# Optimization experiments

Measured on AMD Instinct MI355X. Metric: run time of the kernel, lower is better.

Reference implementation:

```python
import jax, jax.numpy as jnp
import numpy as np

L = 4        # num decoder layers
H = 8        # heads
D = 512      # d_model
DFF = 2048   # ffn hidden
V = 8000     # target vocab
B = 16       # batch
S_ENC = 128  # encoder seq len
T = 32       # decode target_length
START, END, NULL = 1, 2, 0
NEG = -1e9
EPS = 1e-6


def sinusoid_pos(max_len, d):
    pos = np.arange(max_len)[:, None].astype(np.float32)
    i = np.arange(d)[None, :].astype(np.float32)
    ang = pos / np.power(10000.0, (2.0 * np.floor(i / 2.0)) / d)
    pe = np.where(np.arange(d)[None, :] % 2 == 0, np.sin(ang), np.cos(ang))
    return jnp.asarray(pe[None], jnp.float32)  # [1, max_len, d]


def setup_inputs() -> dict:
    key = jax.random.key(0)
    ks = jax.random.split(key, 16)
    g = lambda k, shape: jax.random.normal(k, shape, jnp.float32) * 0.02
    return {
        "target_length": T,
        "encoder_output": jax.random.normal(ks[0], (B, S_ENC, D), jnp.float32),
        "padding_mask": jnp.zeros((B, S_ENC), jnp.float32),  # 1.0 where padded
        "embed": g(ks[1], (V, D)),
        "wq": g(ks[2], (L, D, D)), "wk": g(ks[3], (L, D, D)),
        "wv": g(ks[4], (L, D, D)), "wo": g(ks[5], (L, D, D)),
        "cwq": g(ks[6], (L, D, D)), "cwk": g(ks[7], (L, D, D)),
        "cwv": g(ks[8], (L, D, D)), "cwo": g(ks[9], (L, D, D)),
        "w1": g(ks[10], (L, D, DFF)), "b1": jnp.zeros((L, DFF), jnp.float32),
        "w2": g(ks[11], (L, DFF, D)), "b2": jnp.zeros((L, D), jnp.float32),
        "ln_g": jnp.ones((L, 3, D), jnp.float32), "ln_b": jnp.zeros((L, 3, D), jnp.float32),
        "fc_w": g(ks[12], (D, V)), "fc_b": jnp.zeros((V,), jnp.float32),
    }


def ln(x, g, b):
    m = jnp.mean(x, axis=-1, keepdims=True)
    v = jnp.mean(jnp.square(x - m), axis=-1, keepdims=True)
    return (x - m) * jax.lax.rsqrt(v + EPS) * g + b


def mha(q_in, kv_in, wq, wk, wv, wo, mask):
    Bn, Sq, d = q_in.shape
    dh = d // H
    q = (q_in @ wq).reshape(Bn, Sq, H, dh)
    k = (kv_in @ wk).reshape(Bn, -1, H, dh)
    v = (kv_in @ wv).reshape(Bn, -1, H, dh)
    s = jnp.einsum('bqhd,bkhd->bhqk', q, k) / jnp.sqrt(jnp.float32(dh)) + mask
    a = jax.nn.softmax(s, axis=-1)
    o = jnp.einsum('bhqk,bkhd->bqhd', a, v).reshape(Bn, Sq, d)
    return o @ wo


def decoder_stack(x, encoder_output, self_mask, cross_mask,
                  wq, wk, wv, wo, cwq, cwk, cwv, cwo,
                  w1, b1, w2, b2, ln_g, ln_b):
    for i in range(L):
        a = mha(x, x, wq[i], wk[i], wv[i], wo[i], self_mask)
        x = ln(x + a, ln_g[i, 0], ln_b[i, 0])
        a2 = mha(x, encoder_output, cwq[i], cwk[i], cwv[i], cwo[i], cross_mask)
        x = ln(x + a2, ln_g[i, 1], ln_b[i, 1])
        f = jax.nn.relu(x @ w1[i] + b1[i]) @ w2[i] + b2[i]
        x = ln(x + f, ln_g[i, 2], ln_b[i, 2])
    return x


def reference(target_length, encoder_output, padding_mask, embed,
              wq, wk, wv, wo, cwq, cwk, cwv, cwo,
              w1, b1, w2, b2, ln_g, ln_b, fc_w, fc_b):
    Bn, S, d = encoder_output.shape
    Tp1 = target_length + 1
    pos_enc = sinusoid_pos(Tp1, d)
    sqrt_d = jnp.sqrt(jnp.float32(d))
    cross_mask = padding_mask[:, None, None, :] * NEG  # [B,1,1,S_enc]
    tokens0 = jnp.full((Bn, Tp1), NULL, jnp.int32).at[:, 0].set(START)
    done0 = jnp.zeros((Bn,), bool)

    def step(carry, t):
        tokens, done = carry
        # re-embed the whole (fixed-size, masked) prefix buffer each step
        x = embed[tokens] * sqrt_d + pos_enc
        # only positions <= t are valid keys; no look-ahead mask (matches original)
        self_mask = jnp.where(jnp.arange(Tp1) <= t, 0.0, NEG)[None, None, None, :]
        x = decoder_stack(x, encoder_output, self_mask, cross_mask,
                          wq, wk, wv, wo, cwq, cwk, cwv, cwo,
                          w1, b1, w2, b2, ln_g, ln_b)
        out = x[:, t, :] @ fc_w + fc_b  # logits at last valid position
        max_idx = jnp.argmax(out, axis=-1).astype(jnp.int32)
        done = done | (max_idx == END)
        tok = jnp.where(done, jnp.int32(NULL), max_idx)
        tokens = tokens.at[:, t + 1].set(tok)
        return (tokens, done), None

    (tokens, done), _ = jax.lax.scan(step, (tokens0, done0), jnp.arange(target_length))
    return tokens[:, 1:].astype(jnp.int64)
```

## Files before the change

### kernel.cpp

```cpp
#include <hip/hip_runtime.h>
#include <math.h>

#define L_   4
#define H_   8
#define D_   512
#define DH   64
#define DFF_ 2048
#define V_   8000
#define B_   16
#define SENC 128
#define T_   32
#define TP1  33
#define NEGV -1e9f
#define EPSV 1e-6f
#define SQRTD 22.627416997969522f
#define XSZ  ((size_t)TP1 * B_ * D_)

__global__ __launch_bounds__(256) void gemm32_k(
    const float* __restrict__ A, const float* __restrict__ W,
    const float* __restrict__ bias, float* __restrict__ C,
    int M, int N, int K, int kchunk, size_t pstride, int relu, int tmode)
{
    __shared__ __align__(16) float As[2][16][34];
    __shared__ __align__(16) float Bs[2][16][68];
    int tid = threadIdx.x;
    int tx = tid & 15, ty = tid >> 4;
    int m0 = blockIdx.y * 32, n0 = blockIdx.x * 64;
    int kbeg = blockIdx.z * kchunk;
    int niter = kchunk >> 4;
    C += (size_t)blockIdx.z * pstride;
    int am = tid >> 2, aseg = tid & 3;
    int bk = tid >> 4, bc4 = (tid & 15) * 4;
    float4 aReg = make_float4(0.f, 0.f, 0.f, 0.f), bReg;
    {
        int k0 = kbeg;
        if (tid < 128) {
            int gm = m0 + am;
            if (gm < M) aReg = *(const float4*)&A[(size_t)gm * K + k0 + aseg * 4];
        }
        bReg = *(const float4*)&W[(size_t)(k0 + bk) * N + n0 + bc4];
    }
    if (tid < 128) {
        As[0][aseg * 4 + 0][am] = aReg.x;
        As[0][aseg * 4 + 1][am] = aReg.y;
        As[0][aseg * 4 + 2][am] = aReg.z;
        As[0][aseg * 4 + 3][am] = aReg.w;
    }
    *(float4*)&Bs[0][bk][bc4] = bReg;
    __syncthreads();
    float acc[2][4] = {};
    for (int it = 0; it < niter; it++) {
        int cur = it & 1;
        if (it + 1 < niter) {
            int k0 = kbeg + (it + 1) * 16;
            if (tid < 128) {
                int gm = m0 + am;
                aReg = make_float4(0.f, 0.f, 0.f, 0.f);
                if (gm < M) aReg = *(const float4*)&A[(size_t)gm * K + k0 + aseg * 4];
            }
            bReg = *(const float4*)&W[(size_t)(k0 + bk) * N + n0 + bc4];
        }
        #pragma unroll
        for (int kk = 0; kk < 16; kk++) {
            float2 a2 = *(const float2*)&As[cur][kk][ty * 2];
            float4 b4 = *(const float4*)&Bs[cur][kk][tx * 4];
            acc[0][0] += a2.x * b4.x; acc[0][1] += a2.x * b4.y;
            acc[0][2] += a2.x * b4.z; acc[0][3] += a2.x * b4.w;
            acc[1][0] += a2.y * b4.x; acc[1][1] += a2.y * b4.y;
            acc[1][2] += a2.y * b4.z; acc[1][3] += a2.y * b4.w;
        }
        if (it + 1 < niter) {
            int nxt = 1 - cur;
            if (tid < 128) {
                As[nxt][aseg * 4 + 0][am] = aReg.x;
                As[nxt][aseg * 4 + 1][am] = aReg.y;
                As[nxt][aseg * 4 + 2][am] = aReg.z;
                As[nxt][aseg * 4 + 3][am] = aReg.w;
            }
            *(float4*)&Bs[nxt][bk][bc4] = bReg;
        }
        __syncthreads();
    }
    #pragma unroll
    for (int i = 0; i < 2; i++) {
        int gm = m0 + ty * 2 + i;
        if (gm >= M) continue;
        #pragma unroll
        for (int j = 0; j < 4; j++) {
            int gn = n0 + tx * 4 + j;
            float vv = acc[i][j];
            if (bias) vv += bias[gn];
            if (relu) vv = fmaxf(vv, 0.f);
            if (tmode == 1)
                C[(size_t)(gm >> 7) * 65536 + (size_t)gn * SENC + (gm & 127)] = vv;
            else
                C[(size_t)gm * N + gn] = vv;
        }
    }
}

__global__ __launch_bounds__(256) void gemm_qkv_k(
    const float* __restrict__ A, const float* __restrict__ W0,
    const float* __restrict__ W1, const float* __restrict__ W2,
    float* __restrict__ Cb, int M)
{
    __shared__ __align__(16) float As[2][16][34];
    __shared__ __align__(16) float Bs[2][16][68];
    int sel = blockIdx.x >> 3;
    const float* W = (sel == 0) ? W0 : ((sel == 1) ? W1 : W2);
    float* C = Cb + (size_t)sel * XSZ;
    int tid = threadIdx.x;
    int tx = tid & 15, ty = tid >> 4;
    int m0 = blockIdx.y * 32, n0 = (blockIdx.x & 7) * 64;
    int am = tid >> 2, aseg = tid & 3;
    int bk = tid >> 4, bc4 = (tid & 15) * 4;
    float4 aReg = make_float4(0.f, 0.f, 0.f, 0.f), bReg;
    {
        if (tid < 128) {
            int gm = m0 + am;
            if (gm < M) aReg = *(const float4*)&A[(size_t)gm * D_ + aseg * 4];
        }
        bReg = *(const float4*)&W[(size_t)bk * D_ + n0 + bc4];
    }
    if (tid < 128) {
        As[0][aseg * 4 + 0][am] = aReg.x;
        As[0][aseg * 4 + 1][am] = aReg.y;
        As[0][aseg * 4 + 2][am] = aReg.z;
        As[0][aseg * 4 + 3][am] = aReg.w;
    }
    *(float4*)&Bs[0][bk][bc4] = bReg;
    __syncthreads();
    float acc[2][4] = {};
    for (int it = 0; it < 32; it++) {
        int cur = it & 1;
        if (it + 1 < 32) {
            int k0 = (it + 1) * 16;
            if (tid < 128) {
                int gm = m0 + am;
                aReg = make_float4(0.f, 0.f, 0.f, 0.f);
                if (gm < M) aReg = *(const float4*)&A[(size_t)gm * D_ + k0 + aseg * 4];
            }
            bReg = *(const float4*)&W[(size_t)(k0 + bk) * D_ + n0 + bc4];
        }
        #pragma unroll
        for (int kk = 0; kk < 16; kk++) {
            float2 a2 = *(const float2*)&As[cur][kk][ty * 2];
            float4 b4 = *(const float4*)&Bs[cur][kk][tx * 4];
            acc[0][0] += a2.x * b4.x; acc[0][1] += a2.x * b4.y;
            acc[0][2] += a2.x * b4.z; acc[0][3] += a2.x * b4.w;
            acc[1][0] += a2.y * b4.x; acc[1][1] += a2.y * b4.y;
            acc[1][2] += a2.y * b4.z; acc[1][3] += a2.y * b4.w;
        }
        if (it + 1 < 32) {
            int nxt = 1 - cur;
            if (tid < 128) {
                As[nxt][aseg * 4 + 0][am] = aReg.x;
                As[nxt][aseg * 4 + 1][am] = aReg.y;
                As[nxt][aseg * 4 + 2][am] = aReg.z;
                As[nxt][aseg * 4 + 3][am] = aReg.w;
            }
            *(float4*)&Bs[nxt][bk][bc4] = bReg;
        }
        __syncthreads();
    }
    #pragma unroll
    for (int i = 0; i < 2; i++) {
        int gm = m0 + ty * 2 + i;
        if (gm >= M) continue;
        #pragma unroll
        for (int j = 0; j < 4; j++) {
            int gn = n0 + tx * 4 + j;
            if (sel == 1)
                C[(size_t)(gm & 15) * 16896 + (size_t)gn * TP1 + (gm >> 4)] =
                    acc[i][j];
            else
                C[(size_t)gm * D_ + gn] = acc[i][j];
        }
    }
}

__global__ void init_k(int* __restrict__ tokens, int* __restrict__ done,
                       float* __restrict__ cmask, const float* __restrict__ pm)
{
    int tid = threadIdx.x + blockIdx.x * 256;
    if (tid < B_ * TP1) tokens[tid] = ((tid % TP1) == 0) ? 1 : 0;
    if (tid < B_) done[tid] = 0;
    if (tid < B_ * SENC) cmask[tid] = pm[tid] * NEGV;
}

__global__ __launch_bounds__(256) void pe_k(float* __restrict__ pe)
{
    int p = blockIdx.x;
    for (int d = threadIdx.x; d < D_; d += 256) {
        float fd = (float)(2 * (d / 2)) / (float)D_;
        float ang = (float)p / powf(10000.f, fd);
        pe[(size_t)p * D_ + d] = (d & 1) ? cosf(ang) : sinf(ang);
    }
}

__global__ __launch_bounds__(256) void embed_k(
    const float* __restrict__ embed, int* __restrict__ tokens,
    float* __restrict__ x, const float* __restrict__ pe,
    const float* __restrict__ cand_v, const int* __restrict__ cand_i,
    int* __restrict__ done, int t)
{
    int p = blockIdx.x;
    int b = blockIdx.y;
    int tid = threadIdx.x;
    __shared__ float sv[128];
    __shared__ int si[128];
    __shared__ int stok;
    if (p == t && t > 0) {
        if (tid < 128) {
            float val = -1e30f; int idx = 0x7fffffff;
            if (tid < 125) {
                val = cand_v[(size_t)b * 125 + tid];
                idx = cand_i[(size_t)b * 125 + tid];
            }
            sv[tid] = val; si[tid] = idx;
        }
        __syncthreads();
        for (int s = 64; s; s >>= 1) {
            if (tid < s) {
                float ov = sv[tid + s]; int oi = si[tid + s];
                if (ov > sv[tid] || (ov == sv[tid] && oi < si[tid])) {
                    sv[tid] = ov; si[tid] = oi;
                }
            }
            __syncthreads();
        }
        if (tid == 0) {
            int best = si[0];
            int dn = done[b] | (best == 2 ? 1 : 0);
            done[b] = dn;
            int tk = dn ? 0 : best;
            tokens[b * TP1 + t] = tk;
            stok = tk;
        }
        __syncthreads();
    }
    int tok = (p == t && t > 0) ? stok : tokens[b * TP1 + p];
    const float* e = embed + (size_t)tok * D_;
    const float* pr = pe + (size_t)p * D_;
    float* xr = x + ((size_t)p * B_ + b) * D_;
    int c0 = tid * 2;
    float2 ev = *(const float2*)&e[c0];
    float2 pv = *(const float2*)&pr[c0];
    float2 o;
    o.x = ev.x * SQRTD + pv.x;
    o.y = ev.y * SQRTD + pv.y;
    *(float2*)&xr[c0] = o;
}

__device__ __forceinline__ float block_sum(float s) {
    __shared__ float red[4];
    #pragma unroll
    for (int off = 32; off; off >>= 1) s += __shfl_xor(s, off);
    if ((threadIdx.x & 63) == 0) red[threadIdx.x >> 6] = s;
    __syncthreads();
    float tot = red[0] + red[1] + red[2] + red[3];
    __syncthreads();
    return tot;
}

__device__ __forceinline__ float4 block_sum4(float4 s) {
    __shared__ __align__(16) float red4[4][4];
    #pragma unroll
    for (int off = 32; off; off >>= 1) {
        s.x += __shfl_xor(s.x, off);
        s.y += __shfl_xor(s.y, off);
        s.z += __shfl_xor(s.z, off);
        s.w += __shfl_xor(s.w, off);
    }
    if ((threadIdx.x & 63) == 0) *(float4*)red4[threadIdx.x >> 6] = s;
    __syncthreads();
    float4 t;
    t.x = red4[0][0] + red4[1][0] + red4[2][0] + red4[3][0];
    t.y = red4[0][1] + red4[1][1] + red4[2][1] + red4[3][1];
    t.z = red4[0][2] + red4[1][2] + red4[2][2] + red4[3][2];
    t.w = red4[0][3] + red4[1][3] + red4[2][3] + red4[3][3];
    __syncthreads();
    return t;
}

__global__ __launch_bounds__(256) void attn_mega_k(
    const float* __restrict__ q, const float* __restrict__ kT,
    const float* __restrict__ v, const float* __restrict__ wo,
    const float* __restrict__ KcT, const float* __restrict__ Vc,
    const float* __restrict__ cmask, const float* __restrict__ cwq,
    const float* __restrict__ cwo, float* __restrict__ x,
    const float* __restrict__ lg, const float* __restrict__ lb, int P)
{
    int b = blockIdx.x;
    int p0 = blockIdx.y * 4;
    int tid = threadIdx.x;
    int c0 = tid * 2;
    __shared__ float xs[4][D_];
    __shared__ float arow[4][D_];
    __shared__ float scs[4][H_][SENC + 4];
    __shared__ float inv[4][H_];
    #pragma unroll
    for (int g = 0; g < 4; g++) {
        float2 qv = make_float2(0.f, 0.f);
        if (p0 + g < P)
            qv = *(const float2*)&q[((size_t)(p0 + g) * B_ + b) * D_ + c0];
        *(float2*)&arow[g][c0] = qv;
    }
    __syncthreads();
    {
        int h = tid >> 5, kp = tid & 31;
        float a0 = 0.f, a1 = 0.f, a2 = 0.f, a3 = 0.f;
        if (kp < P) {
            const float* kb = kT + ((size_t)(b * 8 + h) * 64) * TP1 + kp;
            #pragma unroll 8
            for (int d = 0; d < 64; d++) {
                float kv = kb[(size_t)d * TP1];
                a0 += arow[0][h * 64 + d] * kv;
                a1 += arow[1][h * 64 + d] * kv;
                a2 += arow[2][h * 64 + d] * kv;
                a3 += arow[3][h * 64 + d] * kv;
            }
        }
        scs[0][h][kp] = a0 * 0.125f;
        scs[1][h][kp] = a1 * 0.125f;
        scs[2][h][kp] = a2 * 0.125f;
        scs[3][h][kp] = a3 * 0.125f;
    }
    __syncthreads();
    {
        int gh = tid >> 3, lane8 = tid & 7;
        int g = gh >> 3, h = gh & 7;
        float mx = -1e30f;
        for (int j = lane8; j < P; j += 8) mx = fmaxf(mx, scs[g][h][j]);
        mx = fmaxf(mx, __shfl_xor(mx, 1));
        mx = fmaxf(mx, __shfl_xor(mx, 2));
        mx = fmaxf(mx, __shfl_xor(mx, 4));
        float sum = 0.f;
        for (int j = lane8; j < P; j += 8) {
            float e = expf(scs[g][h][j] - mx);
            scs[g][h][j] = e;
            sum += e;
        }
        sum += __shfl_xor(sum, 1);
        sum += __shfl_xor(sum, 2);
        sum += __shfl_xor(sum, 4);
        if (lane8 == 0) inv[g][h] = 1.f / sum;
    }
    __syncthreads();
    {
        int h = tid >> 5;
        float o0[4] = {0.f, 0.f, 0.f, 0.f}, o1[4] = {0.f, 0.f, 0.f, 0.f};
        for (int j = 0; j < P; j++) {
            float2 vv = *(const float2*)&v[((size_t)j * B_ + b) * D_ + c0];
            #pragma unroll
            for (int g = 0; g < 4; g++) {
                float w = scs[g][h][j];
                o0[g] += w * vv.x; o1[g] += w * vv.y;
            }
        }
        #pragma unroll
        for (int g = 0; g < 4; g++) {
            arow[g][c0]     = o0[g] * inv[g][h];
            arow[g][c0 + 1] = o1[g] * inv[g][h];
        }
    }
    __syncthreads();
    {
        float v0[4], v1[4];
        #pragma unroll
        for (int g = 0; g < 4; g++) {
            float2 xv = make_float2(0.f, 0.f);
            if (p0 + g < P)
                xv = *(const float2*)&x[((size_t)(p0 + g) * B_ + b) * D_ + c0];
            v0[g] = xv.x; v1[g] = xv.y;
        }
        #pragma unroll 8
        for (int k = 0; k < D_; k++) {
            float2 wv = *(const float2*)&wo[(size_t)k * D_ + c0];
            #pragma unroll
            for (int g = 0; g < 4; g++) {
                float a = arow[g][k];
                v0[g] += a * wv.x; v1[g] += a * wv.y;
            }
        }
        float4 s1 = make_float4(v0[0] + v1[0], v0[1] + v1[1],
                                v0[2] + v1[2], v0[3] + v1[3]);
        float4 m4 = block_sum4(s1);
        float mean[4] = {m4.x * (1.f / 512.f), m4.y * (1.f / 512.f),
                         m4.z * (1.f / 512.f), m4.w * (1.f / 512.f)};
        float d0[4], d1[4];
        #pragma unroll
        for (int g = 0; g < 4; g++) {
            d0[g] = v0[g] - mean[g]; d1[g] = v1[g] - mean[g];
        }
        float4 s2 = make_float4(d0[0] * d0[0] + d1[0] * d1[0],
                                d0[1] * d0[1] + d1[1] * d1[1],
                                d0[2] * d0[2] + d1[2] * d1[2],
                                d0[3] * d0[3] + d1[3] * d1[3]);
        float4 w4 = block_sum4(s2);
        float var[4] = {w4.x * (1.f / 512.f), w4.y * (1.f / 512.f),
                        w4.z * (1.f / 512.f), w4.w * (1.f / 512.f)};
        float g0 = lg[c0], g1 = lg[c0 + 1];
        float bb0 = lb[c0], bb1 = lb[c0 + 1];
        #pragma unroll
        for (int g = 0; g < 4; g++) {
            float rs = rsqrtf(var[g] + EPSV);
            xs[g][c0]     = d0[g] * rs * g0 + bb0;
            xs[g][c0 + 1] = d1[g] * rs * g1 + bb1;
        }
    }
    __syncthreads();
    {
        float q0[4] = {0.f, 0.f, 0.f, 0.f}, q1[4] = {0.f, 0.f, 0.f, 0.f};
        #pragma unroll 8
        for (int k = 0; k < D_; k++) {
            float2 wv = *(const float2*)&cwq[(size_t)k * D_ + c0];
            #pragma unroll
            for (int g = 0; g < 4; g++) {
                float a = xs[g][k];
                q0[g] += a * wv.x; q1[g] += a * wv.y;
            }
        }
        #pragma unroll
        for (int g = 0; g < 4; g++) {
            arow[g][c0] = q0[g]; arow[g][c0 + 1] = q1[g];
        }
    }
    __syncthreads();
    #pragma unroll
    for (int i = 0; i < 4; i++) {
        int idx = tid + i * 256;
        int h = idx >> 7, s = idx & 127;
        const float* kb = KcT + ((size_t)(b * 512 + h * 64)) * SENC + s;
        float a0 = 0.f, a1 = 0.f, a2 = 0.f, a3 = 0.f;
        #pragma unroll 8
        for (int d = 0; d < 64; d++) {
            float kc = kb[(size_t)d * SENC];
            a0 += arow[0][h * 64 + d] * kc;
            a1 += arow[1][h * 64 + d] * kc;
            a2 += arow[2][h * 64 + d] * kc;
            a3 += arow[3][h * 64 + d] * kc;
        }
        float cm = cmask[b * SENC + s];
        scs[0][h][s] = a0 * 0.125f + cm;
        scs[1][h][s] = a1 * 0.125f + cm;
        scs[2][h][s] = a2 * 0.125f + cm;
        scs[3][h][s] = a3 * 0.125f + cm;
    }
    __syncthreads();
    {
        int gh = tid >> 3, lane8 = tid & 7;
        int g = gh >> 3, h = gh & 7;
        float mx = -1e30f;
        for (int s = lane8; s < SENC; s += 8) mx = fmaxf(mx, scs[g][h][s]);
        mx = fmaxf(mx, __shfl_xor(mx, 1));
        mx = fmaxf(mx, __shfl_xor(mx, 2));
        mx = fmaxf(mx, __shfl_xor(mx, 4));
        float sum = 0.f;
        for (int s = lane8; s < SENC; s += 8) {
            float e = expf(scs[g][h][s] - mx);
            scs[g][h][s] = e;
            sum += e;
        }
        sum += __shfl_xor(sum, 1);
        sum += __shfl_xor(sum, 2);
        sum += __shfl_xor(sum, 4);
        if (lane8 == 0) inv[g][h] = 1.f / sum;
    }
    __syncthreads();
    {
        int h = tid >> 5;
        float o0[4] = {0.f, 0.f, 0.f, 0.f}, o1[4] = {0.f, 0.f, 0.f, 0.f};
        for (int s = 0; s < SENC; s++) {
            float2 vv = *(const float2*)&Vc[((size_t)b * SENC + s) * D_ + c0];
            #pragma unroll
            for (int g = 0; g < 4; g++) {
                float w = scs[g][h][s];
                o0[g] += w * vv.x; o1[g] += w * vv.y;
            }
        }
        #pragma unroll
        for (int g = 0; g < 4; g++) {
            arow[g][c0]     = o0[g] * inv[g][h];
            arow[g][c0 + 1] = o1[g] * inv[g][h];
        }
    }
    __syncthreads();
    {
        float v0[4], v1[4];
        #pragma unroll
        for (int g = 0; g < 4; g++) {
            v0[g] = xs[g][c0]; v1[g] = xs[g][c0 + 1];
        }
        #pragma unroll 8
        for (int k = 0; k < D_; k++) {
            float2 wv = *(const float2*)&cwo[(size_t)k * D_ + c0];
            #pragma unroll
            for (int g = 0; g < 4; g++) {
                float a = arow[g][k];
                v0[g] += a * wv.x; v1[g] += a * wv.y;
            }
        }
        float4 s1 = make_float4(v0[0] + v1[0], v0[1] + v1[1],
                                v0[2] + v1[2], v0[3] + v1[3]);
        float4 m4 = block_sum4(s1);
        float mean[4] = {m4.x * (1.f / 512.f), m4.y * (1.f / 512.f),
                         m4.z * (1.f / 512.f), m4.w * (1.f / 512.f)};
        float d0[4], d1[4];
        #pragma unroll
        for (int g = 0; g < 4; g++) {
            d0[g] = v0[g] - mean[g]; d1[g] = v1[g] - mean[g];
        }
        float4 s2 = make_float4(d0[0] * d0[0] + d1[0] * d1[0],
                                d0[1] * d0[1] + d1[1] * d1[1],
                                d0[2] * d0[2] + d1[2] * d1[2],
                                d0[3] * d0[3] + d1[3] * d1[3]);
        float4 w4 = block_sum4(s2);
        float var[4] = {w4.x * (1.f / 512.f), w4.y * (1.f / 512.f),
                        w4.z * (1.f / 512.f), w4.w * (1.f / 512.f)};
        float g0 = lg[D_ + c0], g1 = lg[D_ + c0 + 1];
        float bb0 = lb[D_ + c0], bb1 = lb[D_ + c0 + 1];
        #pragma unroll
        for (int g = 0; g < 4; g++) {
            if (p0 + g < P) {
                float rs = rsqrtf(var[g] + EPSV);
                float* xr = x + ((size_t)(p0 + g) * B_ + b) * D_;
                xr[c0]     = d0[g] * rs * g0 + bb0;
                xr[c0 + 1] = d1[g] * rs * g1 + bb1;
            }
        }
    }
}

__global__ __launch_bounds__(256) void ln_red_k(
    float* __restrict__ x, const float* __restrict__ parts, size_t pstride,
    int nparts, const float* __restrict__ bias,
    const float* __restrict__ gam, const float* __restrict__ bet)
{
    int r = blockIdx.x;
    float* xr = x + (size_t)r * D_;
    int tid = threadIdx.x;
    float v0 = xr[tid];
    float v1 = xr[tid + 256];
    for (int s = 0; s < nparts; s++) {
        const float* pr = parts + (size_t)s * pstride + (size_t)r * D_;
        v0 += pr[tid];
        v1 += pr[tid + 256];
    }
    if (bias) { v0 += bias[tid]; v1 += bias[tid + 256]; }
    float mean = block_sum(v0 + v1) * (1.f / 512.f);
    float d0 = v0 - mean, d1 = v1 - mean;
    float var = block_sum(d0 * d0 + d1 * d1) * (1.f / 512.f);
    float rs = rsqrtf(var + EPSV);
    xr[tid]       = d0 * rs * gam[tid] + bet[tid];
    xr[tid + 256] = d1 * rs * gam[tid + 256] + bet[tid + 256];
}

__global__ __launch_bounds__(256) void logits_k(
    const float* __restrict__ x, const float* __restrict__ fcw,
    const float* __restrict__ fcb, float* __restrict__ cand_v,
    int* __restrict__ cand_i, int t)
{
    __shared__ float xs[B_][D_];
    __shared__ float red[4][64][B_];
    int tid = threadIdx.x;
    for (int i = tid; i < B_ * D_; i += 256) {
        int b = i >> 9, d = i & 511;
        xs[b][d] = x[((size_t)t * B_ + b) * D_ + d];
    }
    __syncthreads();
    int lane = tid & 63, ks = tid >> 6;
    int col = blockIdx.x * 64 + lane;
    float acc[B_] = {};
    int kb = ks * 128;
    for (int k = kb; k < kb + 128; k++) {
        float w = fcw[(size_t)k * V_ + col];
        #pragma unroll
        for (int b = 0; b < B_; b++) acc[b] += xs[b][k] * w;
    }
    #pragma unroll
    for (int b = 0; b < B_; b++) red[ks][lane][b] = acc[b];
    __syncthreads();
    if (ks == 0) {
        float bias = fcb[col];
        #pragma unroll
        for (int b = 0; b < B_; b++) {
            float val = red[0][lane][b] + red[1][lane][b]
                      + red[2][lane][b] + red[3][lane][b] + bias;
            int idx = col;
            #pragma unroll
            for (int off = 32; off; off >>= 1) {
                float ov = __shfl_down(val, off);
                int oi = __shfl_down(idx, off);
                if (ov > val || (ov == val && oi < idx)) { val = ov; idx = oi; }
            }
            if (lane == 0) {
                cand_v[(size_t)b * 125 + blockIdx.x] = val;
                cand_i[(size_t)b * 125 + blockIdx.x] = idx;
            }
        }
    }
}

__global__ __launch_bounds__(128) void writeout_k(
    const int* __restrict__ tokens, const float* __restrict__ cand_v,
    const int* __restrict__ cand_i, const int* __restrict__ done,
    int* __restrict__ out)
{
    int b = blockIdx.x;
    int tid = threadIdx.x;
    __shared__ float sv[128];
    __shared__ int si[128];
    __shared__ int stok;
    float val = -1e30f; int idx = 0x7fffffff;
    if (tid < 125) {
        val = cand_v[(size_t)b * 125 + tid];
        idx = cand_i[(size_t)b * 125 + tid];
    }
    sv[tid] = val; si[tid] = idx;
    __syncthreads();
    for (int s = 64; s; s >>= 1) {
        if (tid < s) {
            float ov = sv[tid + s]; int oi = si[tid + s];
            if (ov > sv[tid] || (ov == sv[tid] && oi < si[tid])) {
                sv[tid] = ov; si[tid] = oi;
            }
        }
        __syncthreads();
    }
    if (tid == 0) {
        int best = si[0];
        int dn = done[b] | (best == 2 ? 1 : 0);
        stok = dn ? 0 : best;
    }
    __syncthreads();
    if (tid < T_)
        out[b * T_ + tid] = (tid == T_ - 1) ? stok : tokens[b * TP1 + tid + 1];
}

extern "C" void kernel_launch(void* const* d_in, const int* in_sizes, int n_in,
                              void* d_out, int out_size, void* d_ws, size_t ws_size,
                              hipStream_t stream)
{
    const float* enc   = (const float*)d_in[1];
    const float* pm    = (const float*)d_in[2];
    const float* embed = (const float*)d_in[3];
    const float* wq    = (const float*)d_in[4];
    const float* wk    = (const float*)d_in[5];
    const float* wv    = (const float*)d_in[6];
    const float* wo    = (const float*)d_in[7];
    const float* cwq   = (const float*)d_in[8];
    const float* cwk   = (const float*)d_in[9];
    const float* cwv   = (const float*)d_in[10];
    const float* cwo   = (const float*)d_in[11];
    const float* w1    = (const float*)d_in[12];
    const float* b1    = (const float*)d_in[13];
    const float* w2    = (const float*)d_in[14];
    const float* b2    = (const float*)d_in[15];
    const float* ln_g  = (const float*)d_in[16];
    const float* ln_b  = (const float*)d_in[17];
    const float* fcw   = (const float*)d_in[18];
    const float* fcb   = (const float*)d_in[19];

    float* ws = (float*)d_ws;
    size_t off = 0;
    float* x     = ws + off; off += XSZ;
    float* qkv   = ws + off; off += 3 * XSZ;
    float* parts = ws + off; off += 4 * XSZ;
    float* ffnh  = ws + off; off += (size_t)TP1 * B_ * DFF_;
    float* cand_v= ws + off; off += (size_t)B_ * 125;
    float* KcT   = ws + off; off += (size_t)L_ * B_ * SENC * D_;
    float* Vc    = ws + off; off += (size_t)L_ * B_ * SENC * D_;
    float* cmask = ws + off; off += (size_t)B_ * SENC;
    float* pe    = ws + off; off += (size_t)TP1 * D_;
    int* cand_i  = (int*)(ws + off); off += (size_t)B_ * 125;
    int* tokens  = (int*)(ws + off); off += (B_ * TP1 + 63) & ~63;
    int* done    = (int*)(ws + off); off += 64;

    init_k<<<8, 256, 0, stream>>>(tokens, done, cmask, pm);
    pe_k<<<TP1, 256, 0, stream>>>(pe);

    const size_t KVL = (size_t)B_ * SENC * D_;
    for (int l = 0; l < L_; l++) {
        gemm32_k<<<dim3(8, (B_ * SENC) / 32), 256, 0, stream>>>(
            enc, cwk + (size_t)l * D_ * D_, nullptr, KcT + l * KVL,
            B_ * SENC, D_, D_, D_, 0, 0, 1);
        gemm32_k<<<dim3(8, (B_ * SENC) / 32), 256, 0, stream>>>(
            enc, cwv + (size_t)l * D_ * D_, nullptr, Vc + l * KVL,
            B_ * SENC, D_, D_, D_, 0, 0, 0);
    }

    for (int t = 0; t < T_; t++) {
        int P = t + 1;
        int M = P * B_;
        int mt = (M + 31) / 32;

        embed_k<<<dim3(P, B_), 256, 0, stream>>>(
            embed, tokens, x, pe, cand_v, cand_i, done, t);

        for (int l = 0; l < L_; l++) {
            const size_t lw = (size_t)l * D_ * D_;
            gemm_qkv_k<<<dim3(24, mt), 256, 0, stream>>>(
                x, wq + lw, wk + lw, wv + lw, qkv, M);
            attn_mega_k<<<dim3(B_, (P + 3) / 4), 256, 0, stream>>>(
                qkv, qkv + XSZ, qkv + 2 * XSZ, wo + lw,
                KcT + l * KVL, Vc + l * KVL, cmask, cwq + lw, cwo + lw, x,
                ln_g + (size_t)(l * 3 + 0) * D_, ln_b + (size_t)(l * 3 + 0) * D_, P);
            gemm32_k<<<dim3(32, mt), 256, 0, stream>>>(
                x, w1 + (size_t)l * D_ * DFF_, b1 + (size_t)l * DFF_, ffnh,
                M, DFF_, D_, D_, 0, 1, 0);
            gemm32_k<<<dim3(8, mt, 4), 256, 0, stream>>>(
                ffnh, w2 + (size_t)l * DFF_ * D_, nullptr, parts,
                M, D_, DFF_, 512, XSZ, 0, 0);
            ln_red_k<<<M, 256, 0, stream>>>(x, parts, XSZ, 4, b2 + (size_t)l * D_,
                ln_g + (size_t)(l * 3 + 2) * D_, ln_b + (size_t)(l * 3 + 2) * D_);
        }

        logits_k<<<V_ / 64, 256, 0, stream>>>(x, fcw, fcb, cand_v, cand_i, t);
    }

    writeout_k<<<B_, 128, 0, stream>>>(tokens, cand_v, cand_i, done, (int*)d_out);
}
```

Before: 24.24 ms.

## Enlarge GEMM tiles to 32x128 with 4x8 register blocking and 128 threads

Both fp32 GEMM kernels move from 32x64 tiles on 256 threads to 32x128 tiles on 128 threads. Each thread now computes a 4x8 micro-tile, loads A with float4 from shared memory, and writes the non-transposed outputs as float4. The aim is more arithmetic per shared-memory load and fewer idle threads. The trade-off is half as many blocks, which hurts parallelism on the small-M decode steps that dominate here. Separately, the logits kernel drops its shared-memory staging of x and reads activations straight from global memory through the cache.

```diff
diff --git a/kernel.cpp b/kernel.cpp
--- a/kernel.cpp
+++ b/kernel.cpp
@@ -16,165 +16,226 @@
 #define SQRTD 22.627416997969522f
 #define XSZ  ((size_t)TP1 * B_ * D_)
 
-__global__ __launch_bounds__(256) void gemm32_k(
+__global__ __launch_bounds__(128) void gemm32_k(
     const float* __restrict__ A, const float* __restrict__ W,
     const float* __restrict__ bias, float* __restrict__ C,
     int M, int N, int K, int kchunk, size_t pstride, int relu, int tmode)
 {
-    __shared__ __align__(16) float As[2][16][34];
-    __shared__ __align__(16) float Bs[2][16][68];
+    __shared__ __align__(16) float As[2][16][36];
+    __shared__ __align__(16) float Bs[2][16][132];
     int tid = threadIdx.x;
     int tx = tid & 15, ty = tid >> 4;
-    int m0 = blockIdx.y * 32, n0 = blockIdx.x * 64;
+    int m0 = blockIdx.y * 32, n0 = blockIdx.x * 128;
     int kbeg = blockIdx.z * kchunk;
     int niter = kchunk >> 4;
     C += (size_t)blockIdx.z * pstride;
     int am = tid >> 2, aseg = tid & 3;
-    int bk = tid >> 4, bc4 = (tid & 15) * 4;
-    float4 aReg = make_float4(0.f, 0.f, 0.f, 0.f), bReg;
-    {
-        int k0 = kbeg;
-        if (tid < 128) {
-            int gm = m0 + am;
-            if (gm < M) aReg = *(const float4*)&A[(size_t)gm * K + k0 + aseg * 4];
-        }
-        bReg = *(const float4*)&W[(size_t)(k0 + bk) * N + n0 + bc4];
-    }
-    if (tid < 128) {
-        As[0][aseg * 4 + 0][am] = aReg.x;
-        As[0][aseg * 4 + 1][am] = aReg.y;
-        As[0][aseg * 4 + 2][am] = aReg.z;
-        As[0][aseg * 4 + 3][am] = aReg.w;
-    }
-    *(float4*)&Bs[0][bk][bc4] = bReg;
-    __syncthreads();
-    float acc[2][4] = {};
+    int bk = tid >> 3, bc4 = (tid & 7) * 4;
+    float4 aReg = make_float4(0.f, 0.f, 0.f, 0.f), bReg[4];
+    {
+        int gm = m0 + am;
+        if (gm < M) aReg = *(const float4*)&A[(size_t)gm * K + kbeg + aseg * 4];
+        const float* wr = &W[(size_t)(kbeg + bk) * N + n0 + bc4];
+        bReg[0] = *(const float4*)&wr[0];
+        bReg[1] = *(const float4*)&wr[32];
+        bReg[2] = *(const float4*)&wr[64];
+        bReg[3] = *(const float4*)&wr[96];
+    }
+    As[0][aseg * 4 + 0][am] = aReg.x;
+    As[0][aseg * 4 + 1][am] = aReg.y;
+    As[0][aseg * 4 + 2][am] = aReg.z;
+    As[0][aseg * 4 + 3][am] = aReg.w;
+    *(float4*)&Bs[0][bk][bc4]      = bReg[0];
+    *(float4*)&Bs[0][bk][bc4 + 32] = bReg[1];
+    *(float4*)&Bs[0][bk][bc4 + 64] = bReg[2];
+    *(float4*)&Bs[0][bk][bc4 + 96] = bReg[3];
+    __syncthreads();
+    float acc[4][8] = {};
     for (int it = 0; it < niter; it++) {
         int cur = it & 1;
         if (it + 1 < niter) {
             int k0 = kbeg + (it + 1) * 16;
-            if (tid < 128) {
-                int gm = m0 + am;
-                aReg = make_float4(0.f, 0.f, 0.f, 0.f);
-                if (gm < M) aReg = *(const float4*)&A[(size_t)gm * K + k0 + aseg * 4];
-            }
-            bReg = *(const float4*)&W[(size_t)(k0 + bk) * N + n0 + bc4];
+            int gm = m0 + am;
+            aReg = make_float4(0.f, 0.f, 0.f, 0.f);
+            if (gm < M) aReg = *(const float4*)&A[(size_t)gm * K + k0 + aseg * 4];
+            const float* wr = &W[(size_t)(k0 + bk) * N + n0 + bc4];
+            bReg[0] = *(const float4*)&wr[0];
+            bReg[1] = *(const float4*)&wr[32];
+            bReg[2] = *(const float4*)&wr[64];
+            bReg[3] = *(const float4*)&wr[96];
         }
         #pragma unroll
         for (int kk = 0; kk < 16; kk++) {
-            float2 a2 = *(const float2*)&As[cur][kk][ty * 2];
+            float4 a4 = *(const float4*)&As[cur][kk][ty * 4];
             float4 b4 = *(const float4*)&Bs[cur][kk][tx * 4];
-            acc[0][0] += a2.x * b4.x; acc[0][1] += a2.x * b4.y;
-            acc[0][2] += a2.x * b4.z; acc[0][3] += a2.x * b4.w;
-            acc[1][0] += a2.y * b4.x; acc[1][1] += a2.y * b4.y;
-            acc[1][2] += a2.y * b4.z; acc[1][3] += a2.y * b4.w;
+            float4 c4 = *(const float4*)&Bs[cur][kk][tx * 4 + 64];
+            acc[0][0] += a4.x * b4.x; acc[0][1] += a4.x * b4.y;
+            acc[0][2] += a4.x * b4.z; acc[0][3] += a4.x * b4.w;
+            acc[0][4] += a4.x * c4.x; acc[0][5] += a4.x * c4.y;
+            acc[0][6] += a4.x * c4.z; acc[0][7] += a4.x * c4.w;
+            acc[1][0] += a4.y * b4.x; acc[1][1] += a4.y * b4.y;
+            acc[1][2] += a4.y * b4.z; acc[1][3] += a4.y * b4.w;
+            acc[1][4] += a4.y * c4.x; acc[1][5] += a4.y * c4.y;
+            acc[1][6] += a4.y * c4.z; acc[1][7] += a4.y * c4.w;
+            acc[2][0] += a4.z * b4.x; acc[2][1] += a4.z * b4.y;
+            acc[2][2] += a4.z * b4.z; acc[2][3] += a4.z * b4.w;
+            acc[2][4] += a4.z * c4.x; acc[2][5] += a4.z * c4.y;
+            acc[2][6] += a4.z * c4.z; acc[2][7] += a4.z * c4.w;
+            acc[3][0] += a4.w * b4.x; acc[3][1] += a4.w * b4.y;
+            acc[3][2] += a4.w * b4.z; acc[3][3] += a4.w * b4.w;
+            acc[3][4] += a4.w * c4.x; acc[3][5] += a4.w * c4.y;
+            acc[3][6] += a4.w * c4.z; acc[3][7] += a4.w * c4.w;
         }
         if (it + 1 < niter) {
             int nxt = 1 - cur;
-            if (tid < 128) {
-                As[nxt][aseg * 4 + 0][am] = aReg.x;
-                As[nxt][aseg * 4 + 1][am] = aReg.y;
-                As[nxt][aseg * 4 + 2][am] = aReg.z;
-                As[nxt][aseg * 4 + 3][am] = aReg.w;
-            }
-            *(float4*)&Bs[nxt][bk][bc4] = bReg;
+            As[nxt][aseg * 4 + 0][am] = aReg.x;
+            As[nxt][aseg * 4 + 1][am] = aReg.y;
+            As[nxt][aseg * 4 + 2][am] = aReg.z;
+            As[nxt][aseg * 4 + 3][am] = aReg.w;
+            *(float4*)&Bs[nxt][bk][bc4]      = bReg[0];
+            *(float4*)&Bs[nxt][bk][bc4 + 32] = bReg[1];
+            *(float4*)&Bs[nxt][bk][bc4 + 64] = bReg[2];
+            *(float4*)&Bs[nxt][bk][bc4 + 96] = bReg[3];
         }
         __syncthreads();
     }
     #pragma unroll
-    for (int i = 0; i < 2; i++) {
-        int gm = m0 + ty * 2 + i;
+    for (int i = 0; i < 4; i++) {
+        int gm = m0 + ty * 4 + i;
         if (gm >= M) continue;
-        #pragma unroll
-        for (int j = 0; j < 4; j++) {
-            int gn = n0 + tx * 4 + j;
-            float vv = acc[i][j];
-            if (bias) vv += bias[gn];
-            if (relu) vv = fmaxf(vv, 0.f);
-            if (tmode == 1)
+        if (tmode == 1) {
+            #pragma unroll
+            for (int j = 0; j < 8; j++) {
+                int gn = n0 + tx * 4 + (j >> 2) * 64 + (j & 3);
+                float vv = acc[i][j];
+                if (bias) vv += bias[gn];
+                if (relu) vv = fmaxf(vv, 0.f);
                 C[(size_t)(gm >> 7) * 65536 + (size_t)gn * SENC + (gm & 127)] = vv;
-            else
-                C[(size_t)gm * N + gn] = vv;
-        }
-    }
-}
-
-__global__ __launch_bounds__(256) void gemm_qkv_k(
+            }
+        } else {
+            int gn = n0 + tx * 4;
+            float4 o0, o1;
+            o0.x = acc[i][0]; o0.y = acc[i][1]; o0.z = acc[i][2]; o0.w = acc[i][3];
+            o1.x = acc[i][4]; o1.y = acc[i][5]; o1.z = acc[i][6]; o1.w = acc[i][7];
+            if (bias) {
+                o0.x += bias[gn + 0];  o0.y += bias[gn + 1];
+                o0.z += bias[gn + 2];  o0.w += bias[gn + 3];
+                o1.x += bias[gn + 64]; o1.y += bias[gn + 65];
+                o1.z += bias[gn + 66]; o1.w += bias[gn + 67];
+            }
+            if (relu) {
+                o0.x = fmaxf(o0.x, 0.f); o0.y = fmaxf(o0.y, 0.f);
+                o0.z = fmaxf(o0.z, 0.f); o0.w = fmaxf(o0.w, 0.f);
+                o1.x = fmaxf(o1.x, 0.f); o1.y = fmaxf(o1.y, 0.f);
+                o1.z = fmaxf(o1.z, 0.f); o1.w = fmaxf(o1.w, 0.f);
+            }
+            *(float4*)&C[(size_t)gm * N + gn]      = o0;
+            *(float4*)&C[(size_t)gm * N + gn + 64] = o1;
+        }
+    }
+}
+
+__global__ __launch_bounds__(128) void gemm_qkv_k(
     const float* __restrict__ A, const float* __restrict__ W0,
     const float* __restrict__ W1, const float* __restrict__ W2,
     float* __restrict__ Cb, int M)
 {
-    __shared__ __align__(16) float As[2][16][34];
-    __shared__ __align__(16) float Bs[2][16][68];
-    int sel = blockIdx.x >> 3;
+    __shared__ __align__(16) float As[2][16][36];
+    __shared__ __align__(16) float Bs[2][16][132];
+    int sel = blockIdx.x >> 2;
     const float* W = (sel == 0) ? W0 : ((sel == 1) ? W1 : W2);
     float* C = Cb + (size_t)sel * XSZ;
     int tid = threadIdx.x;
     int tx = tid & 15, ty = tid >> 4;
-    int m0 = blockIdx.y * 32, n0 = (blockIdx.x & 7) * 64;
+    int m0 = blockIdx.y * 32, n0 = (blockIdx.x & 3) * 128;
     int am = tid >> 2, aseg = tid & 3;
-    int bk = tid >> 4, bc4 = (tid & 15) * 4;
-    float4 aReg = make_float4(0.f, 0.f, 0.f, 0.f), bReg;
-    {
-        if (tid < 128) {
-            int gm = m0 + am;
-            if (gm < M) aReg = *(const float4*)&A[(size_t)gm * D_ + aseg * 4];
-        }
-        bReg = *(const float4*)&W[(size_t)bk * D_ + n0 + bc4];
-    }
-    if (tid < 128) {
-        As[0][aseg * 4 + 0][am] = aReg.x;
-        As[0][aseg * 4 + 1][am] = aReg.y;
-        As[0][aseg * 4 + 2][am] = aReg.z;
-        As[0][aseg * 4 + 3][am] = aReg.w;
-    }
-    *(float4*)&Bs[0][bk][bc4] = bReg;
-    __syncthreads();
-    float acc[2][4] = {};
+    int bk = tid >> 3, bc4 = (tid & 7) * 4;
+    float4 aReg = make_float4(0.f, 0.f, 0.f, 0.f), bReg[4];
+    {
+        int gm = m0 + am;
+        if (gm < M) aReg = *(const float4*)&A[(size_t)gm * D_ + aseg * 4];
+        const float* wr = &W[(size_t)bk * D_ + n0 + bc4];
+        bReg[0] = *(const float4*)&wr[0];
+        bReg[1] = *(const float4*)&wr[32];
+        bReg[2] = *(const float4*)&wr[64];
+        bReg[3] = *(const float4*)&wr[96];
+    }
+    As[0][aseg * 4 + 0][am] = aReg.x;
+    As[0][aseg * 4 + 1][am] = aReg.y;
+    As[0][aseg * 4 + 2][am] = aReg.z;
+    As[0][aseg * 4 + 3][am] = aReg.w;
+    *(float4*)&Bs[0][bk][bc4]      = bReg[0];
+    *(float4*)&Bs[0][bk][bc4 + 32] = bReg[1];
+    *(float4*)&Bs[0][bk][bc4 + 64] = bReg[2];
+    *(float4*)&Bs[0][bk][bc4 + 96] = bReg[3];
+    __syncthreads();
+    float acc[4][8] = {};
     for (int it = 0; it < 32; it++) {
         int cur = it & 1;
         if (it + 1 < 32) {
             int k0 = (it + 1) * 16;
-            if (tid < 128) {
-                int gm = m0 + am;
-                aReg = make_float4(0.f, 0.f, 0.f, 0.f);
-                if (gm < M) aReg = *(const float4*)&A[(size_t)gm * D_ + k0 + aseg * 4];
-            }
-            bReg = *(const float4*)&W[(size_t)(k0 + bk) * D_ + n0 + bc4];
+            int gm = m0 + am;
+            aReg = make_float4(0.f, 0.f, 0.f, 0.f);
+            if (gm < M) aReg = *(const float4*)&A[(size_t)gm * D_ + k0 + aseg * 4];
+            const float* wr = &W[(size_t)(k0 + bk) * D_ + n0 + bc4];
+            bReg[0] = *(const float4*)&wr[0];
+            bReg[1] = *(const float4*)&wr[32];
+            bReg[2] = *(const float4*)&wr[64];
+            bReg[3] = *(const float4*)&wr[96];
         }
         #pragma unroll
         for (int kk = 0; kk < 16; kk++) {
-            float2 a2 = *(const float2*)&As[cur][kk][ty * 2];
+            float4 a4 = *(const float4*)&As[cur][kk][ty * 4];
             float4 b4 = *(const float4*)&Bs[cur][kk][tx * 4];
-            acc[0][0] += a2.x * b4.x; acc[0][1] += a2.x * b4.y;
-            acc[0][2] += a2.x * b4.z; acc[0][3] += a2.x * b4.w;
-            acc[1][0] += a2.y * b4.x; acc[1][1] += a2.y * b4.y;
-            acc[1][2] += a2.y * b4.z; acc[1][3] += a2.y * b4.w;
+            float4 c4 = *(const float4*)&Bs[cur][kk][tx * 4 + 64];
+            acc[0][0] += a4.x * b4.x; acc[0][1] += a4.x * b4.y;
+            acc[0][2] += a4.x * b4.z; acc[0][3] += a4.x * b4.w;
+            acc[0][4] += a4.x * c4.x; acc[0][5] += a4.x * c4.y;
+            acc[0][6] += a4.x * c4.z; acc[0][7] += a4.x * c4.w;
+            acc[1][0] += a4.y * b4.x; acc[1][1] += a4.y * b4.y;
+            acc[1][2] += a4.y * b4.z; acc[1][3] += a4.y * b4.w;
+            acc[1][4] += a4.y * c4.x; acc[1][5] += a4.y * c4.y;
+            acc[1][6] += a4.y * c4.z; acc[1][7] += a4.y * c4.w;
+            acc[2][0] += a4.z * b4.x; acc[2][1] += a4.z * b4.y;
+            acc[2][2] += a4.z * b4.z; acc[2][3] += a4.z * b4.w;
+            acc[2][4] += a4.z * c4.x; acc[2][5] += a4.z * c4.y;
+            acc[2][6] += a4.z * c4.z; acc[2][7] += a4.z * c4.w;
+            acc[3][0] += a4.w * b4.x; acc[3][1] += a4.w * b4.y;
+            acc[3][2] += a4.w * b4.z; acc[3][3] += a4.w * b4.w;
+            acc[3][4] += a4.w * c4.x; acc[3][5] += a4.w * c4.y;
+            acc[3][6] += a4.w * c4.z; acc[3][7] += a4.w * c4.w;
         }
         if (it + 1 < 32) {
             int nxt = 1 - cur;
-            if (tid < 128) {
-                As[nxt][aseg * 4 + 0][am] = aReg.x;
-                As[nxt][aseg * 4 + 1][am] = aReg.y;
-                As[nxt][aseg * 4 + 2][am] = aReg.z;
-                As[nxt][aseg * 4 + 3][am] = aReg.w;
-            }
-            *(float4*)&Bs[nxt][bk][bc4] = bReg;
+            As[nxt][aseg * 4 + 0][am] = aReg.x;
+            As[nxt][aseg * 4 + 1][am] = aReg.y;
+            As[nxt][aseg * 4 + 2][am] = aReg.z;
+            As[nxt][aseg * 4 + 3][am] = aReg.w;
+            *(float4*)&Bs[nxt][bk][bc4]      = bReg[0];
+            *(float4*)&Bs[nxt][bk][bc4 + 32] = bReg[1];
+            *(float4*)&Bs[nxt][bk][bc4 + 64] = bReg[2];
+            *(float4*)&Bs[nxt][bk][bc4 + 96] = bReg[3];
         }
         __syncthreads();
     }
     #pragma unroll
-    for (int i = 0; i < 2; i++) {
-        int gm = m0 + ty * 2 + i;
+    for (int i = 0; i < 4; i++) {
+        int gm = m0 + ty * 4 + i;
         if (gm >= M) continue;
-        #pragma unroll
-        for (int j = 0; j < 4; j++) {
-            int gn = n0 + tx * 4 + j;
-            if (sel == 1)
+        if (sel == 1) {
+            #pragma unroll
+            for (int j = 0; j < 8; j++) {
+                int gn = n0 + tx * 4 + (j >> 2) * 64 + (j & 3);
                 C[(size_t)(gm & 15) * 16896 + (size_t)gn * TP1 + (gm >> 4)] =
                     acc[i][j];
-            else
-                C[(size_t)gm * D_ + gn] = acc[i][j];
+            }
+        } else {
+            int gn = n0 + tx * 4;
+            float4 o0, o1;
+            o0.x = acc[i][0]; o0.y = acc[i][1]; o0.z = acc[i][2]; o0.w = acc[i][3];
+            o1.x = acc[i][4]; o1.y = acc[i][5]; o1.z = acc[i][6]; o1.w = acc[i][7];
+            *(float4*)&C[(size_t)gm * D_ + gn]      = o0;
+            *(float4*)&C[(size_t)gm * D_ + gn + 64] = o1;
         }
     }
 }
@@ -561,22 +622,17 @@
     const float* __restrict__ fcb, float* __restrict__ cand_v,
     int* __restrict__ cand_i, int t)
 {
-    __shared__ float xs[B_][D_];
     __shared__ float red[4][64][B_];
     int tid = threadIdx.x;
-    for (int i = tid; i < B_ * D_; i += 256) {
-        int b = i >> 9, d = i & 511;
-        xs[b][d] = x[((size_t)t * B_ + b) * D_ + d];
-    }
-    __syncthreads();
     int lane = tid & 63, ks = tid >> 6;
     int col = blockIdx.x * 64 + lane;
+    const float* xr = x + (size_t)t * B_ * D_;
     float acc[B_] = {};
     int kb = ks * 128;
     for (int k = kb; k < kb + 128; k++) {
         float w = fcw[(size_t)k * V_ + col];
         #pragma unroll
-        for (int b = 0; b < B_; b++) acc[b] += xs[b][k] * w;
+        for (int b = 0; b < B_; b++) acc[b] += xr[(size_t)b * D_ + k] * w;
     }
     #pragma unroll
     for (int b = 0; b < B_; b++) red[ks][lane][b] = acc[b];
@@ -682,10 +738,10 @@
 
     const size_t KVL = (size_t)B_ * SENC * D_;
     for (int l = 0; l < L_; l++) {
-        gemm32_k<<<dim3(8, (B_ * SENC) / 32), 256, 0, stream>>>(
+        gemm32_k<<<dim3(4, (B_ * SENC) / 32), 128, 0, stream>>>(
             enc, cwk + (size_t)l * D_ * D_, nullptr, KcT + l * KVL,
             B_ * SENC, D_, D_, D_, 0, 0, 1);
-        gemm32_k<<<dim3(8, (B_ * SENC) / 32), 256, 0, stream>>>(
+        gemm32_k<<<dim3(4, (B_ * SENC) / 32), 128, 0, stream>>>(
             enc, cwv + (size_t)l * D_ * D_, nullptr, Vc + l * KVL,
             B_ * SENC, D_, D_, D_, 0, 0, 0);
     }
@@ -700,16 +756,16 @@
 
         for (int l = 0; l < L_; l++) {
             const size_t lw = (size_t)l * D_ * D_;
-            gemm_qkv_k<<<dim3(24, mt), 256, 0, stream>>>(
+            gemm_qkv_k<<<dim3(12, mt), 128, 0, stream>>>(
                 x, wq + lw, wk + lw, wv + lw, qkv, M);
             attn_mega_k<<<dim3(B_, (P + 3) / 4), 256, 0, stream>>>(
                 qkv, qkv + XSZ, qkv + 2 * XSZ, wo + lw,
                 KcT + l * KVL, Vc + l * KVL, cmask, cwq + lw, cwo + lw, x,
                 ln_g + (size_t)(l * 3 + 0) * D_, ln_b + (size_t)(l * 3 + 0) * D_, P);
-            gemm32_k<<<dim3(32, mt), 256, 0, stream>>>(
+            gemm32_k<<<dim3(16, mt), 128, 0, stream>>>(
                 x, w1 + (size_t)l * D_ * DFF_, b1 + (size_t)l * DFF_, ffnh,
                 M, DFF_, D_, D_, 0, 1, 0);
-            gemm32_k<<<dim3(8, mt, 4), 256, 0, stream>>>(
+            gemm32_k<<<dim3(4, mt, 4), 128, 0, stream>>>(
                 ffnh, w2 + (size_t)l * DFF_ * D_, nullptr, parts,
                 M, D_, DFF_, 512, XSZ, 0, 0);
             ln_red_k<<<M, 256, 0, stream>>>(x, parts, XSZ, 4, b2 + (size_t)l * D_,
```

Result: slower. 34.10 ms (+40.7%).
